# Kernel optimization log

Measured on AMD Instinct MI355X. Metric: run time of the kernel, lower is better.

Reference implementation:

```python
import jax, jax.numpy as jnp
import numpy as np

B, LAT, H, OUT, S, L = 256, 128, 256, 64, 512, 2


def _lstm_layer(xs, h0, c0, Wih, Whh, bih, bhh):
    # xs: [B, S, in_dim]; PyTorch gate order i, f, g, o
    gx = jnp.einsum('bsi,gi->bsg', xs, Wih) + bih + bhh  # [B,S,4H], precomputed input proj
    gx = jnp.swapaxes(gx, 0, 1)  # [S,B,4H]

    def step(carry, g_t):
        h, c = carry
        g = g_t + h @ Whh.T
        i, f, gg, o = jnp.split(g, 4, axis=-1)
        i, f, o = jax.nn.sigmoid(i), jax.nn.sigmoid(f), jax.nn.sigmoid(o)
        c = f * c + i * jnp.tanh(gg)
        h = o * jnp.tanh(c)
        return (h, c), h

    (_, _), hs = jax.lax.scan(step, (h0, c0), gx)
    return jnp.swapaxes(hs, 0, 1)  # [B,S,H]


def setup_inputs() -> dict:
    key = jax.random.key(0)
    ks = jax.random.split(key, 20)
    sc = 0.05
    d = {
        'z': jax.random.normal(ks[0], (B, LAT), jnp.float32),
        'fc_hidden_w': jax.random.normal(ks[1], (H * L, LAT), jnp.float32) * sc,
        'fc_hidden_b': jnp.zeros((H * L,), jnp.float32),
        'fc_cell_w': jax.random.normal(ks[2], (H * L, LAT), jnp.float32) * sc,
        'fc_cell_b': jnp.zeros((H * L,), jnp.float32),
        'fc_input_w': jax.random.normal(ks[3], (H, LAT), jnp.float32) * sc,
        'fc_input_b': jnp.zeros((H,), jnp.float32),
        'W_ih0': jax.random.normal(ks[4], (4 * H, H), jnp.float32) * sc,
        'W_hh0': jax.random.normal(ks[5], (4 * H, H), jnp.float32) * sc,
        'b_ih0': jnp.zeros((4 * H,), jnp.float32),
        'b_hh0': jnp.zeros((4 * H,), jnp.float32),
        'W_ih1': jax.random.normal(ks[6], (4 * H, H), jnp.float32) * sc,
        'W_hh1': jax.random.normal(ks[7], (4 * H, H), jnp.float32) * sc,
        'b_ih1': jnp.zeros((4 * H,), jnp.float32),
        'b_hh1': jnp.zeros((4 * H,), jnp.float32),
        'fc_output_w': jax.random.normal(ks[8], (OUT, H), jnp.float32) * sc,
        'fc_output_b': jnp.zeros((OUT,), jnp.float32),
    }
    return d


def reference(z, fc_hidden_w, fc_hidden_b, fc_cell_w, fc_cell_b, fc_input_w, fc_input_b,
              W_ih0, W_hh0, b_ih0, b_hh0, W_ih1, W_hh1, b_ih1, b_hh1,
              fc_output_w, fc_output_b):
    # init hidden/cell per layer: view(B, L, H) -> layer axis first
    hidden = (z @ fc_hidden_w.T + fc_hidden_b).reshape(B, L, H)
    cell = (z @ fc_cell_w.T + fc_cell_b).reshape(B, L, H)
    # repeated decoder input (same vector at every timestep)
    x0 = z @ fc_input_w.T + fc_input_b  # [B,H]
    xs = jnp.broadcast_to(x0[:, None, :], (B, S, H))
    h1 = _lstm_layer(xs, hidden[:, 0], cell[:, 0], W_ih0, W_hh0, b_ih0, b_hh0)
    # dropout between layers is inference no-op
    h2 = _lstm_layer(h1, hidden[:, 1], cell[:, 1], W_ih1, W_hh1, b_ih1, b_hh1)
    return h2 @ fc_output_w.T + fc_output_b  # [B,S,OUT]
```

## Files before the change

### kernel.cpp

```cpp
#include <hip/hip_runtime.h>
#include <hip/hip_bf16.h>

#define LAT 128
#define H 256
#define OUTD 64
#define SEQ 512

typedef short bf16x8 __attribute__((ext_vector_type(8)));
typedef float f32x4  __attribute__((ext_vector_type(4)));
typedef unsigned long long u64;
typedef unsigned u32;

__device__ __forceinline__ float sigm(float x)  { return 1.f / (1.f + __expf(-x)); }
__device__ __forceinline__ float tanhf_(float x){ return 1.f - 2.f / (__expf(2.f * x) + 1.f); }

__device__ __forceinline__ short f2bs(float x) {
    __hip_bfloat16 b = __float2bfloat16(x);
    return *reinterpret_cast<short*>(&b);
}
__device__ __forceinline__ float bs2f(unsigned short h) {
    u32 b = ((u32)h) << 16;
    float f; __builtin_memcpy(&f, &b, 4); return f;
}
__device__ __forceinline__ u32 f2pair(float a, float b) {
    return ((u32)(unsigned short)f2bs(b) << 16) | (u32)(unsigned short)f2bs(a);
}
__device__ __forceinline__ bf16x8 pack8(const float* s) {
    bf16x8 v;
    v[0]=f2bs(s[0]); v[1]=f2bs(s[1]); v[2]=f2bs(s[2]); v[3]=f2bs(s[3]);
    v[4]=f2bs(s[4]); v[5]=f2bs(s[5]); v[6]=f2bs(s[6]); v[7]=f2bs(s[7]);
    return v;
}

__device__ __forceinline__ u64 sys_load_u64(const u64* p) {
    return __hip_atomic_load((u64*)p, __ATOMIC_RELAXED, __HIP_MEMORY_SCOPE_SYSTEM);
}
__device__ __forceinline__ void sys_store_u64(u64* p, u64 v) {
    __hip_atomic_store(p, v, __ATOMIC_RELAXED, __HIP_MEMORY_SCOPE_SYSTEM);
}

__global__ void lstm_prologue_init(const float* __restrict__ z,
                                   const float* __restrict__ Whid,
                                   const float* __restrict__ bhid,
                                   const float* __restrict__ Wcell,
                                   const float* __restrict__ bcell,
                                   const float* __restrict__ bih1,
                                   const float* __restrict__ bhh1,
                                   u64* __restrict__ h0B1,
                                   u64* __restrict__ h1B1,
                                   float* __restrict__ c0,
                                   float* __restrict__ c1,
                                   float* __restrict__ gxb1)
{
    int t = blockIdx.x * 256 + threadIdx.x;
    if (t < 65536) {
        int layer = t >> 15;
        int tt = t & 32767;
        int b = tt >> 7, cp = tt & 127;
        int colA = layer * H + 2 * cp;
        const float* zr = z + b * LAT;
        const float* wA = Whid + colA * LAT;
        const float* wB = wA + LAT;
        float a0 = bhid[colA], a1 = bhid[colA + 1];
        for (int k = 0; k < LAT; k++) { float zv = zr[k]; a0 += zv * wA[k]; a1 += zv * wB[k]; }
        u64 v = ((u64)(u32)layer << 32) | (u64)f2pair(a0, a1);
        (layer ? h1B1 : h0B1)[b * 128 + cp] = v;
    } else if (t < 196608) {
        int tt = t - 65536;
        int b = tt >> 9, col = tt & 511;
        const float* w  = Wcell + col * LAT;
        const float* zr = z + b * LAT;
        float acc = bcell[col];
        for (int k = 0; k < LAT; k++) acc += zr[k] * w[k];
        if (col < H) c0[b * H + col] = acc;
        else         c1[b * H + (col - H)] = acc;
    } else if (t < 197632) {
        int g = t - 196608;
        gxb1[g] = bih1[g] + bhh1[g];
    }
}

__global__ void lstm_prologue_gx0(const float* __restrict__ z,
                                  const float* __restrict__ Win,
                                  const float* __restrict__ bin,
                                  const float* __restrict__ Wih0,
                                  const float* __restrict__ bih0,
                                  const float* __restrict__ bhh0,
                                  u32* __restrict__ gxb0u)
{
    __shared__ float xs[H];
    const int b = blockIdx.y;
    const int tid = threadIdx.x;
    {
        const float* w  = Win + tid * LAT;
        const float* zr = z + b * LAT;
        float acc = bin[tid];
        for (int k = 0; k < LAT; k++) acc += zr[k] * w[k];
        xs[tid] = acc;
    }
    __syncthreads();
    const int cA = blockIdx.x * 512 + 2 * tid;
    const float* wA = Wih0 + cA * H;
    const float* wB = wA + H;
    float a0 = bih0[cA]     + bhh0[cA];
    float a1 = bih0[cA + 1] + bhh0[cA + 1];
    for (int k = 0; k < H; k++) { float xv = xs[k]; a0 += xv * wA[k]; a1 += xv * wB[k]; }
    gxb0u[b * 512 + blockIdx.x * 256 + tid] = f2pair(a0, a1);
}

__global__ __launch_bounds__(256, 1)
void lstm_persistent(const u32* __restrict__ gxb0u, const float* __restrict__ gxb1,
                     const float* __restrict__ c0g, const float* __restrict__ c1g,
                     u64* __restrict__ h0B0, u64* __restrict__ h0B1,
                     u64* __restrict__ h1B0, u64* __restrict__ h1B1,
                     const float* __restrict__ Whh0, const float* __restrict__ Wih1,
                     const float* __restrict__ Whh1, const float* __restrict__ Wout,
                     const float* __restrict__ bout, float* __restrict__ out)
{
    const int wg = blockIdx.x;
    const int bg = wg >> 4;
    const int j  = wg & 15;
    const int tid  = threadIdx.x;
    const int wave = tid >> 6;
    const int q  = (tid >> 4) & 3;
    const int ln = tid & 15;
    const int mycol = j * 16 + wave * 4 + q;
    const int myb   = bg * 16 + ln;

    __shared__ u32 hs0[2][16 * 132];
    __shared__ u32 hs1[2][16 * 132];

    bf16x8 wf[3][8];
    {
        const float* mats[3] = { Whh0, Wih1, Whh1 };
        const int arow = (ln & 3) * H + j * 16 + wave * 4 + (ln >> 2);
        #pragma unroll
        for (int mm = 0; mm < 3; mm++) {
            const float* s = mats[mm] + arow * H;
            #pragma unroll
            for (int kk = 0; kk < 8; kk++) wf[mm][kk] = pack8(s + kk * 32 + q * 8);
        }
    }
    const bool doOut = (j < 4) && (wave == 0);
    bf16x8 wo[8];
    float bor[4] = {0.f, 0.f, 0.f, 0.f};
    if (doOut) {
        const int orow = j * 16 + ln;
        const float* s = Wout + orow * H;
        #pragma unroll
        for (int kk = 0; kk < 8; kk++) wo[kk] = pack8(s + kk * 32 + q * 8);
        #pragma unroll
        for (int r = 0; r < 4; r++) bor[r] = bout[j * 16 + q * 4 + r];
    }

    float gxr0[4], gxr1[4];
    #pragma unroll
    for (int r = 0; r < 4; r++) {
        u32 v = gxb0u[myb * 512 + ((r * 256 + mycol) >> 1)];
        gxr0[r] = bs2f((unsigned short)((mycol & 1) ? (v >> 16) : (v & 0xFFFFu)));
        gxr1[r] = gxb1[r * 256 + mycol];
    }
    float creg0 = c0g[myb * H + mycol];
    float creg1 = c1g[myb * H + mycol];

    u64* A0 = h0B0 + bg * 2048;
    u64* A1 = h0B1 + bg * 2048;
    u64* B0 = h1B0 + bg * 2048;
    u64* B1 = h1B1 + bg * 2048;

    const int pubslot = ln * 128 + j * 8 + wave * 2 + (q >> 1);
    const bool pubLane = ((q & 1) == 0);

    u64 v0[8];
    #pragma unroll
    for (int i = 0; i < 8; i++) v0[i] = sys_load_u64(A1 + i * 256 + tid);

    for (int k = 0; k <= SEQ + 1; k++) {
        const u64* P1 = (k & 1) ? B1 : B0;  u64* C1 = (k & 1) ? B0 : B1;
        u64* C0 = (k & 1) ? A1 : A0;
        const int par = k & 1;

        u64 v1[8];
        if (k >= 1) {
            #pragma unroll
            for (int i = 0; i < 8; i++) v1[i] = sys_load_u64(P1 + i * 256 + tid);
        }

        if (k <= SEQ) {
            const u64* P0 = (k & 1) ? A0 : A1;
            bool ok = true;
            #pragma unroll
            for (int i = 0; i < 8; i++) ok = ok && ((u32)(v0[i] >> 32) == (u32)k);
            int guard = 0;
            while (!ok && guard < 16384) {
                ok = true;
                #pragma unroll
                for (int i = 0; i < 8; i++) v0[i] = sys_load_u64(P0 + i * 256 + tid);
                #pragma unroll
                for (int i = 0; i < 8; i++) ok = ok && ((u32)(v0[i] >> 32) == (u32)k);
                guard++;
            }
            u32* dst = hs0[par];
            #pragma unroll
            for (int i = 0; i < 8; i++) { int s = i * 256 + tid; dst[(s >> 7) * 132 + (s & 127)] = (u32)v0[i]; }
        }

        if (k >= 1) {
            bool ok = true;
            #pragma unroll
            for (int i = 0; i < 8; i++) ok = ok && ((u32)(v1[i] >> 32) == (u32)k);
            int guard = 0;
            while (!ok && guard < 16384) {
                ok = true;
                #pragma unroll
                for (int i = 0; i < 8; i++) v1[i] = sys_load_u64(P1 + i * 256 + tid);
                #pragma unroll
                for (int i = 0; i < 8; i++) ok = ok && ((u32)(v1[i] >> 32) == (u32)k);
                guard++;
            }
            u32* dst = hs1[par];
            #pragma unroll
            for (int i = 0; i < 8; i++) { int s = i * 256 + tid; dst[(s >> 7) * 132 + (s & 127)] = (u32)v1[i]; }
        }
        __syncthreads();

        bf16x8 hb0[8];
        {
            const unsigned short* b0p = (const unsigned short*)hs0[par];
            #pragma unroll
            for (int kk = 0; kk < 8; kk++)
                hb0[kk] = *(const bf16x8*)(b0p + ln * 264 + kk * 32 + q * 8);
        }
        bf16x8 hb1[8];
        {
            const unsigned short* b1p = (const unsigned short*)hs1[par];
            #pragma unroll
            for (int kk = 0; kk < 8; kk++)
                hb1[kk] = *(const bf16x8*)(b1p + ln * 264 + kk * 32 + q * 8);
        }

        if (k < SEQ) {
            f32x4 acc = {0.f, 0.f, 0.f, 0.f};
            #pragma unroll
            for (int kk = 0; kk < 8; kk++)
                acc = __builtin_amdgcn_mfma_f32_16x16x32_bf16(wf[0][kk], hb0[kk], acc, 0, 0, 0);
            float i_ = sigm(acc[0] + gxr0[0]);
            float f_ = sigm(acc[1] + gxr0[1]);
            float g_ = tanhf_(acc[2] + gxr0[2]);
            float o_ = sigm(acc[3] + gxr0[3]);
            creg0 = f_ * creg0 + i_ * g_;
            int us = (int)(u32)(unsigned short)f2bs(o_ * tanhf_(creg0));
            int other = __shfl_xor(us, 16);
            if (pubLane) {
                u32 pa = (u32)us | ((u32)other << 16);
                sys_store_u64(C0 + pubslot, ((u64)(u32)(k + 1) << 32) | (u64)pa);
            }
        }

        if (k >= 1 && k <= SEQ) {
            f32x4 acc = {0.f, 0.f, 0.f, 0.f};
            #pragma unroll
            for (int kk = 0; kk < 8; kk++)
                acc = __builtin_amdgcn_mfma_f32_16x16x32_bf16(wf[1][kk], hb0[kk], acc, 0, 0, 0);
            #pragma unroll
            for (int kk = 0; kk < 8; kk++)
                acc = __builtin_amdgcn_mfma_f32_16x16x32_bf16(wf[2][kk], hb1[kk], acc, 0, 0, 0);
            float i_ = sigm(acc[0] + gxr1[0]);
            float f_ = sigm(acc[1] + gxr1[1]);
            float g_ = tanhf_(acc[2] + gxr1[2]);
            float o_ = sigm(acc[3] + gxr1[3]);
            creg1 = f_ * creg1 + i_ * g_;
            int us = (int)(u32)(unsigned short)f2bs(o_ * tanhf_(creg1));
            int other = __shfl_xor(us, 16);
            if (pubLane) {
                u32 pa = (u32)us | ((u32)other << 16);
                sys_store_u64(C1 + pubslot, ((u64)(u32)(k + 1) << 32) | (u64)pa);
            }
        }

        if (k < SEQ) {
            #pragma unroll
            for (int i = 0; i < 8; i++) v0[i] = sys_load_u64(C0 + i * 256 + tid);
        }

        if (k >= 2 && doOut) {
            f32x4 acc = {0.f, 0.f, 0.f, 0.f};
            #pragma unroll
            for (int kk = 0; kk < 8; kk++)
                acc = __builtin_amdgcn_mfma_f32_16x16x32_bf16(wo[kk], hb1[kk], acc, 0, 0, 0);
            f32x4 res;
            #pragma unroll
            for (int r = 0; r < 4; r++) res[r] = acc[r] + bor[r];
            *(f32x4*)&out[(bg * 16 + ln) * (SEQ * OUTD) + (k - 2) * OUTD + j * 16 + q * 4] = res;
        }
    }
}

extern "C" void kernel_launch(void* const* d_in, const int* in_sizes, int n_in,
                              void* d_out, int out_size, void* d_ws, size_t ws_size,
                              hipStream_t stream) {
    const float* z     = (const float*)d_in[0];
    const float* Whid  = (const float*)d_in[1];
    const float* bhid  = (const float*)d_in[2];
    const float* Wcell = (const float*)d_in[3];
    const float* bcell = (const float*)d_in[4];
    const float* Win   = (const float*)d_in[5];
    const float* bin   = (const float*)d_in[6];
    const float* Wih0  = (const float*)d_in[7];
    const float* Whh0  = (const float*)d_in[8];
    const float* bih0  = (const float*)d_in[9];
    const float* bhh0  = (const float*)d_in[10];
    const float* Wih1  = (const float*)d_in[11];
    const float* Whh1  = (const float*)d_in[12];
    const float* bih1  = (const float*)d_in[13];
    const float* bhh1  = (const float*)d_in[14];
    const float* Wout  = (const float*)d_in[15];
    const float* bout  = (const float*)d_in[16];
    float* out = (float*)d_out;

    u32*   gxb0u = (u32*)d_ws;
    float* gxb1  = (float*)(gxb0u + 131072);
    float* c0    = gxb1 + 1024;
    float* c1    = c0 + 65536;
    u64*   h0B0  = (u64*)(c1 + 65536);
    u64*   h0B1  = h0B0 + 32768;
    u64*   h1B0  = h0B1 + 32768;
    u64*   h1B1  = h1B0 + 32768;

    lstm_prologue_init<<<772, 256, 0, stream>>>(z, Whid, bhid, Wcell, bcell,
                                                bih1, bhh1, h0B1, h1B1, c0, c1, gxb1);
    lstm_prologue_gx0<<<dim3(2, 256), 256, 0, stream>>>(z, Win, bin, Wih0, bih0, bhh0, gxb0u);

    void* kargs[] = { (void*)&gxb0u, (void*)&gxb1, (void*)&c0, (void*)&c1,
                      (void*)&h0B0, (void*)&h0B1, (void*)&h1B0, (void*)&h1B1,
                      (void*)&Whh0, (void*)&Wih1, (void*)&Whh1, (void*)&Wout,
                      (void*)&bout, (void*)&out };
    hipError_t ce = hipLaunchCooperativeKernel((const void*)lstm_persistent,
                                               dim3(256), dim3(256), kargs, 0, stream);
    if (ce != hipSuccess) {
        lstm_persistent<<<256, 256, 0, stream>>>(gxb0u, gxb1, c0, c1,
                                                 h0B0, h0B1, h1B0, h1B1,
                                                 Whh0, Wih1, Whh1, Wout, bout, out);
    }
}
```

Baseline: 1.851 ms.

## Split LSTM layers across two wave groups per block and use agent-scope atomics

Each persistent block now runs 512 threads: the first 256 compute layer 0 and the second 256 compute layer 1 plus the output projection, so the two layers' MFMA and gate work run in parallel waves rather than serially in the same threads. Each group polls only its own flag buffer, and the per-thread weight register footprint shrinks. The flag loads and stores also drop from system scope to agent scope, which should make the cross-block handshakes cheaper. The costs are lower register budgets from the 512-thread launch bounds and the need for the cooperative launch to fit 512-thread blocks.

```diff
diff --git a/kernel.cpp b/kernel.cpp
--- a/kernel.cpp
+++ b/kernel.cpp
@@ -33,10 +33,10 @@
 }
 
 __device__ __forceinline__ u64 sys_load_u64(const u64* p) {
-    return __hip_atomic_load((u64*)p, __ATOMIC_RELAXED, __HIP_MEMORY_SCOPE_SYSTEM);
+    return __hip_atomic_load((u64*)p, __ATOMIC_RELAXED, __HIP_MEMORY_SCOPE_AGENT);
 }
 __device__ __forceinline__ void sys_store_u64(u64* p, u64 v) {
-    __hip_atomic_store(p, v, __ATOMIC_RELAXED, __HIP_MEMORY_SCOPE_SYSTEM);
+    __hip_atomic_store(p, v, __ATOMIC_RELAXED, __HIP_MEMORY_SCOPE_AGENT);
 }
 
 __global__ void lstm_prologue_init(const float* __restrict__ z,
@@ -108,7 +108,7 @@
     gxb0u[b * 512 + blockIdx.x * 256 + tid] = f2pair(a0, a1);
 }
 
-__global__ __launch_bounds__(256, 1)
+__global__ __launch_bounds__(512, 2)
 void lstm_persistent(const u32* __restrict__ gxb0u, const float* __restrict__ gxb1,
                      const float* __restrict__ c0g, const float* __restrict__ c1g,
                      u64* __restrict__ h0B0, u64* __restrict__ h0B1,
@@ -120,29 +120,36 @@
     const int wg = blockIdx.x;
     const int bg = wg >> 4;
     const int j  = wg & 15;
-    const int tid  = threadIdx.x;
-    const int wave = tid >> 6;
-    const int q  = (tid >> 4) & 3;
-    const int ln = tid & 15;
-    const int mycol = j * 16 + wave * 4 + q;
+    const int tid = threadIdx.x;
+    const int grp = tid >> 8;
+    const int gt  = tid & 255;
+    const int gwave = gt >> 6;
+    const int q  = (gt >> 4) & 3;
+    const int ln = gt & 15;
+    const int mycol = j * 16 + gwave * 4 + q;
     const int myb   = bg * 16 + ln;
 
     __shared__ u32 hs0[2][16 * 132];
     __shared__ u32 hs1[2][16 * 132];
 
-    bf16x8 wf[3][8];
+    bf16x8 wfA[8], wfB[8], wo[8];
     {
-        const float* mats[3] = { Whh0, Wih1, Whh1 };
-        const int arow = (ln & 3) * H + j * 16 + wave * 4 + (ln >> 2);
-        #pragma unroll
-        for (int mm = 0; mm < 3; mm++) {
-            const float* s = mats[mm] + arow * H;
+        const int arow = (ln & 3) * H + j * 16 + gwave * 4 + (ln >> 2);
+        if (grp == 0) {
+            const float* s = Whh0 + arow * H;
             #pragma unroll
-            for (int kk = 0; kk < 8; kk++) wf[mm][kk] = pack8(s + kk * 32 + q * 8);
+            for (int kk = 0; kk < 8; kk++) wfA[kk] = pack8(s + kk * 32 + q * 8);
+        } else {
+            const float* s1 = Wih1 + arow * H;
+            const float* s2 = Whh1 + arow * H;
+            #pragma unroll
+            for (int kk = 0; kk < 8; kk++) {
+                wfA[kk] = pack8(s1 + kk * 32 + q * 8);
+                wfB[kk] = pack8(s2 + kk * 32 + q * 8);
+            }
         }
     }
-    const bool doOut = (j < 4) && (wave == 0);
-    bf16x8 wo[8];
+    const bool doOut = (grp == 1) && (j < 4) && (gwave == 0);
     float bor[4] = {0.f, 0.f, 0.f, 0.f};
     if (doOut) {
         const int orow = j * 16 + ln;
@@ -153,145 +160,151 @@
         for (int r = 0; r < 4; r++) bor[r] = bout[j * 16 + q * 4 + r];
     }
 
-    float gxr0[4], gxr1[4];
-    #pragma unroll
-    for (int r = 0; r < 4; r++) {
-        u32 v = gxb0u[myb * 512 + ((r * 256 + mycol) >> 1)];
-        gxr0[r] = bs2f((unsigned short)((mycol & 1) ? (v >> 16) : (v & 0xFFFFu)));
-        gxr1[r] = gxb1[r * 256 + mycol];
-    }
-    float creg0 = c0g[myb * H + mycol];
-    float creg1 = c1g[myb * H + mycol];
+    float gxr[4], creg;
+    if (grp == 0) {
+        #pragma unroll
+        for (int r = 0; r < 4; r++) {
+            u32 v = gxb0u[myb * 512 + ((r * 256 + mycol) >> 1)];
+            gxr[r] = bs2f((unsigned short)((mycol & 1) ? (v >> 16) : (v & 0xFFFFu)));
+        }
+        creg = c0g[myb * H + mycol];
+    } else {
+        #pragma unroll
+        for (int r = 0; r < 4; r++) gxr[r] = gxb1[r * 256 + mycol];
+        creg = c1g[myb * H + mycol];
+    }
 
     u64* A0 = h0B0 + bg * 2048;
     u64* A1 = h0B1 + bg * 2048;
     u64* B0 = h1B0 + bg * 2048;
     u64* B1 = h1B1 + bg * 2048;
 
-    const int pubslot = ln * 128 + j * 8 + wave * 2 + (q >> 1);
+    const int pubslot = ln * 128 + j * 8 + gwave * 2 + (q >> 1);
     const bool pubLane = ((q & 1) == 0);
 
-    u64 v0[8];
-    #pragma unroll
-    for (int i = 0; i < 8; i++) v0[i] = sys_load_u64(A1 + i * 256 + tid);
+    u64 v[8];
+    if (grp == 0) {
+        #pragma unroll
+        for (int i = 0; i < 8; i++) v[i] = sys_load_u64(A1 + i * 256 + gt);
+    }
 
     for (int k = 0; k <= SEQ + 1; k++) {
-        const u64* P1 = (k & 1) ? B1 : B0;  u64* C1 = (k & 1) ? B0 : B1;
-        u64* C0 = (k & 1) ? A1 : A0;
         const int par = k & 1;
 
-        u64 v1[8];
-        if (k >= 1) {
-            #pragma unroll
-            for (int i = 0; i < 8; i++) v1[i] = sys_load_u64(P1 + i * 256 + tid);
-        }
-
-        if (k <= SEQ) {
-            const u64* P0 = (k & 1) ? A0 : A1;
-            bool ok = true;
-            #pragma unroll
-            for (int i = 0; i < 8; i++) ok = ok && ((u32)(v0[i] >> 32) == (u32)k);
-            int guard = 0;
-            while (!ok && guard < 16384) {
-                ok = true;
-                #pragma unroll
-                for (int i = 0; i < 8; i++) v0[i] = sys_load_u64(P0 + i * 256 + tid);
-                #pragma unroll
-                for (int i = 0; i < 8; i++) ok = ok && ((u32)(v0[i] >> 32) == (u32)k);
-                guard++;
-            }
-            u32* dst = hs0[par];
-            #pragma unroll
-            for (int i = 0; i < 8; i++) { int s = i * 256 + tid; dst[(s >> 7) * 132 + (s & 127)] = (u32)v0[i]; }
-        }
-
-        if (k >= 1) {
-            bool ok = true;
-            #pragma unroll
-            for (int i = 0; i < 8; i++) ok = ok && ((u32)(v1[i] >> 32) == (u32)k);
-            int guard = 0;
-            while (!ok && guard < 16384) {
-                ok = true;
-                #pragma unroll
-                for (int i = 0; i < 8; i++) v1[i] = sys_load_u64(P1 + i * 256 + tid);
-                #pragma unroll
-                for (int i = 0; i < 8; i++) ok = ok && ((u32)(v1[i] >> 32) == (u32)k);
-                guard++;
-            }
-            u32* dst = hs1[par];
-            #pragma unroll
-            for (int i = 0; i < 8; i++) { int s = i * 256 + tid; dst[(s >> 7) * 132 + (s & 127)] = (u32)v1[i]; }
+        if (grp == 0) {
+            if (k <= SEQ) {
+                const u64* P0 = par ? A0 : A1;
+                bool ok = true;
+                #pragma unroll
+                for (int i = 0; i < 8; i++) ok = ok && ((u32)(v[i] >> 32) == (u32)k);
+                int guard = 0;
+                while (!ok && guard < 16384) {
+                    ok = true;
+                    #pragma unroll
+                    for (int i = 0; i < 8; i++) v[i] = sys_load_u64(P0 + i * 256 + gt);
+                    #pragma unroll
+                    for (int i = 0; i < 8; i++) ok = ok && ((u32)(v[i] >> 32) == (u32)k);
+                    guard++;
+                }
+                u32* dst = hs0[par];
+                #pragma unroll
+                for (int i = 0; i < 8; i++) { int s = i * 256 + gt; dst[(s >> 7) * 132 + (s & 127)] = (u32)v[i]; }
+            }
+        } else {
+            if (k >= 1) {
+                const u64* P1 = par ? B1 : B0;
+                bool ok = true;
+                #pragma unroll
+                for (int i = 0; i < 8; i++) ok = ok && ((u32)(v[i] >> 32) == (u32)k);
+                int guard = 0;
+                while (!ok && guard < 16384) {
+                    ok = true;
+                    #pragma unroll
+                    for (int i = 0; i < 8; i++) v[i] = sys_load_u64(P1 + i * 256 + gt);
+                    #pragma unroll
+                    for (int i = 0; i < 8; i++) ok = ok && ((u32)(v[i] >> 32) == (u32)k);
+                    guard++;
+                }
+                u32* dst = hs1[par];
+                #pragma unroll
+                for (int i = 0; i < 8; i++) { int s = i * 256 + gt; dst[(s >> 7) * 132 + (s & 127)] = (u32)v[i]; }
+            }
         }
         __syncthreads();
 
-        bf16x8 hb0[8];
-        {
-            const unsigned short* b0p = (const unsigned short*)hs0[par];
-            #pragma unroll
-            for (int kk = 0; kk < 8; kk++)
-                hb0[kk] = *(const bf16x8*)(b0p + ln * 264 + kk * 32 + q * 8);
-        }
-        bf16x8 hb1[8];
-        {
-            const unsigned short* b1p = (const unsigned short*)hs1[par];
-            #pragma unroll
-            for (int kk = 0; kk < 8; kk++)
-                hb1[kk] = *(const bf16x8*)(b1p + ln * 264 + kk * 32 + q * 8);
-        }
-
-        if (k < SEQ) {
-            f32x4 acc = {0.f, 0.f, 0.f, 0.f};
-            #pragma unroll
-            for (int kk = 0; kk < 8; kk++)
-                acc = __builtin_amdgcn_mfma_f32_16x16x32_bf16(wf[0][kk], hb0[kk], acc, 0, 0, 0);
-            float i_ = sigm(acc[0] + gxr0[0]);
-            float f_ = sigm(acc[1] + gxr0[1]);
-            float g_ = tanhf_(acc[2] + gxr0[2]);
-            float o_ = sigm(acc[3] + gxr0[3]);
-            creg0 = f_ * creg0 + i_ * g_;
-            int us = (int)(u32)(unsigned short)f2bs(o_ * tanhf_(creg0));
-            int other = __shfl_xor(us, 16);
-            if (pubLane) {
-                u32 pa = (u32)us | ((u32)other << 16);
-                sys_store_u64(C0 + pubslot, ((u64)(u32)(k + 1) << 32) | (u64)pa);
-            }
-        }
-
-        if (k >= 1 && k <= SEQ) {
-            f32x4 acc = {0.f, 0.f, 0.f, 0.f};
-            #pragma unroll
-            for (int kk = 0; kk < 8; kk++)
-                acc = __builtin_amdgcn_mfma_f32_16x16x32_bf16(wf[1][kk], hb0[kk], acc, 0, 0, 0);
-            #pragma unroll
-            for (int kk = 0; kk < 8; kk++)
-                acc = __builtin_amdgcn_mfma_f32_16x16x32_bf16(wf[2][kk], hb1[kk], acc, 0, 0, 0);
-            float i_ = sigm(acc[0] + gxr1[0]);
-            float f_ = sigm(acc[1] + gxr1[1]);
-            float g_ = tanhf_(acc[2] + gxr1[2]);
-            float o_ = sigm(acc[3] + gxr1[3]);
-            creg1 = f_ * creg1 + i_ * g_;
-            int us = (int)(u32)(unsigned short)f2bs(o_ * tanhf_(creg1));
-            int other = __shfl_xor(us, 16);
-            if (pubLane) {
-                u32 pa = (u32)us | ((u32)other << 16);
-                sys_store_u64(C1 + pubslot, ((u64)(u32)(k + 1) << 32) | (u64)pa);
-            }
-        }
-
-        if (k < SEQ) {
-            #pragma unroll
-            for (int i = 0; i < 8; i++) v0[i] = sys_load_u64(C0 + i * 256 + tid);
-        }
-
-        if (k >= 2 && doOut) {
-            f32x4 acc = {0.f, 0.f, 0.f, 0.f};
-            #pragma unroll
-            for (int kk = 0; kk < 8; kk++)
-                acc = __builtin_amdgcn_mfma_f32_16x16x32_bf16(wo[kk], hb1[kk], acc, 0, 0, 0);
-            f32x4 res;
-            #pragma unroll
-            for (int r = 0; r < 4; r++) res[r] = acc[r] + bor[r];
-            *(f32x4*)&out[(bg * 16 + ln) * (SEQ * OUTD) + (k - 2) * OUTD + j * 16 + q * 4] = res;
+        if (grp == 0) {
+            if (k < SEQ) {
+                bf16x8 hb0[8];
+                const unsigned short* p0 = (const unsigned short*)hs0[par];
+                #pragma unroll
+                for (int kk = 0; kk < 8; kk++)
+                    hb0[kk] = *(const bf16x8*)(p0 + ln * 264 + kk * 32 + q * 8);
+                f32x4 acc = {0.f, 0.f, 0.f, 0.f};
+                #pragma unroll
+                for (int kk = 0; kk < 8; kk++)
+                    acc = __builtin_amdgcn_mfma_f32_16x16x32_bf16(wfA[kk], hb0[kk], acc, 0, 0, 0);
+                float i_ = sigm(acc[0] + gxr[0]);
+                float f_ = sigm(acc[1] + gxr[1]);
+                float g_ = tanhf_(acc[2] + gxr[2]);
+                float o_ = sigm(acc[3] + gxr[3]);
+                creg = f_ * creg + i_ * g_;
+                int us = (int)(u32)(unsigned short)f2bs(o_ * tanhf_(creg));
+                int other = __shfl_xor(us, 16);
+                u64* C0 = par ? A1 : A0;
+                if (pubLane) {
+                    u32 pa = (u32)us | ((u32)other << 16);
+                    sys_store_u64(C0 + pubslot, ((u64)(u32)(k + 1) << 32) | (u64)pa);
+                }
+                #pragma unroll
+                for (int i = 0; i < 8; i++) v[i] = sys_load_u64(C0 + i * 256 + gt);
+            }
+        } else {
+            bf16x8 hb1f[8];
+            if (k >= 1) {
+                const unsigned short* p1 = (const unsigned short*)hs1[par];
+                #pragma unroll
+                for (int kk = 0; kk < 8; kk++)
+                    hb1f[kk] = *(const bf16x8*)(p1 + ln * 264 + kk * 32 + q * 8);
+            }
+            if (k >= 1 && k <= SEQ) {
+                bf16x8 hb0[8];
+                const unsigned short* p0 = (const unsigned short*)hs0[par];
+                #pragma unroll
+                for (int kk = 0; kk < 8; kk++)
+                    hb0[kk] = *(const bf16x8*)(p0 + ln * 264 + kk * 32 + q * 8);
+                f32x4 accA = {0.f, 0.f, 0.f, 0.f};
+                f32x4 accB = {0.f, 0.f, 0.f, 0.f};
+                #pragma unroll
+                for (int kk = 0; kk < 8; kk++) {
+                    accA = __builtin_amdgcn_mfma_f32_16x16x32_bf16(wfA[kk], hb0[kk], accA, 0, 0, 0);
+                    accB = __builtin_amdgcn_mfma_f32_16x16x32_bf16(wfB[kk], hb1f[kk], accB, 0, 0, 0);
+                }
+                float i_ = sigm(accA[0] + accB[0] + gxr[0]);
+                float f_ = sigm(accA[1] + accB[1] + gxr[1]);
+                float g_ = tanhf_(accA[2] + accB[2] + gxr[2]);
+                float o_ = sigm(accA[3] + accB[3] + gxr[3]);
+                creg = f_ * creg + i_ * g_;
+                int us = (int)(u32)(unsigned short)f2bs(o_ * tanhf_(creg));
+                int other = __shfl_xor(us, 16);
+                u64* C1 = par ? B0 : B1;
+                if (pubLane) {
+                    u32 pa = (u32)us | ((u32)other << 16);
+                    sys_store_u64(C1 + pubslot, ((u64)(u32)(k + 1) << 32) | (u64)pa);
+                }
+            }
+            if (k <= SEQ) {
+                const u64* C1p = par ? B0 : B1;
+                #pragma unroll
+                for (int i = 0; i < 8; i++) v[i] = sys_load_u64(C1p + i * 256 + gt);
+            }
+            if (doOut && k >= 2) {
+                f32x4 acc;
+                acc[0] = bor[0]; acc[1] = bor[1]; acc[2] = bor[2]; acc[3] = bor[3];
+                #pragma unroll
+                for (int kk = 0; kk < 8; kk++)
+                    acc = __builtin_amdgcn_mfma_f32_16x16x32_bf16(wo[kk], hb1f[kk], acc, 0, 0, 0);
+                *(f32x4*)&out[(bg * 16 + ln) * (SEQ * OUTD) + (k - 2) * OUTD + j * 16 + q * 4] = acc;
+            }
         }
     }
 }
@@ -336,9 +349,9 @@
                       (void*)&Whh0, (void*)&Wih1, (void*)&Whh1, (void*)&Wout,
                       (void*)&bout, (void*)&out };
     hipError_t ce = hipLaunchCooperativeKernel((const void*)lstm_persistent,
-                                               dim3(256), dim3(256), kargs, 0, stream);
+                                               dim3(256), dim3(512), kargs, 0, stream);
     if (ce != hipSuccess) {
-        lstm_persistent<<<256, 256, 0, stream>>>(gxb0u, gxb1, c0, c1,
+        lstm_persistent<<<256, 512, 0, stream>>>(gxb0u, gxb1, c0, c1,
                                                  h0B0, h0B1, h1B0, h1B1,
                                                  Whh0, Wih1, Whh1, Wout, bout, out);
     }
```

Measured after the change: 2.525 ms. +36.4%, slower.
